# Kernel tuning notes

Hardware: AMD Instinct MI355X
Metric: run time of the kernel (lower is better)

The kernel has to match this reference:

```python
import jax, jax.numpy as jnp
import numpy as np

B, L, H, D = 4, 2048, 12, 64
CHUNK = 128  # chunk size for the causal linear-attention scan
EPS = 1e-6


def setup_inputs() -> dict:
    key = jax.random.key(0)
    kq, kk, kv = jax.random.split(key, 3)
    return {
        "q": jax.random.normal(kq, (B, L, H, D), jnp.float32),
        "k": jax.random.normal(kk, (B, L, H, D), jnp.float32),
        "v": jax.random.normal(kv, (B, L, H, D), jnp.float32),
    }


def _phi(x):
    # elu feature map: elu(x) + 1 (strictly positive)
    return jax.nn.elu(x) + 1.0


def _causal_linear(q, k, v):
    """Chunked causal linear attention numerator.
    out[l] = q[l] @ sum_{s<=l} k[s] (x) v[s].  q,k,v: [N,L,H,D]."""
    n, l, h, d = q.shape
    g = l // CHUNK
    qc = q.reshape(n, g, CHUNK, h, d)
    kc = k.reshape(n, g, CHUNK, h, d)
    vc = v.reshape(n, g, CHUNK, h, d)
    # per-chunk kv outer-product sums -> [N, G, H, D, M]
    kv = jnp.einsum('ngchd,ngchm->nghdm', kc, vc)
    # exclusive prefix sum over chunks (state entering each chunk)
    s_incl = jnp.cumsum(kv, axis=1)
    s_excl = jnp.concatenate([jnp.zeros_like(s_incl[:, :1]), s_incl[:, :-1]], axis=1)
    inter = jnp.einsum('ngchd,nghdm->ngchm', qc, s_excl)
    # intra-chunk causal part
    scores = jnp.einsum('ngchd,ngshd->ngchs', qc, kc)  # [N,G,C,H,C]
    mask = jnp.tril(jnp.ones((CHUNK, CHUNK), scores.dtype))  # s <= c
    scores = scores * mask.reshape(1, 1, CHUNK, 1, CHUNK)
    intra = jnp.einsum('ngchs,ngshm->ngchm', scores, vc)
    return (inter + intra).reshape(n, l, h, -1)


def reference(q, k, v):
    qf = _phi(q)
    kf = _phi(k)
    # normalizer z[n,l,h] = q[l] . cumsum_s<=l k[s]
    z = jnp.einsum('nlhd,nlhd->nlh', qf, jnp.cumsum(kf, axis=1)) + EPS
    num = _causal_linear(qf, kf, v)
    return num / z[..., None]
```

## Files before the change

### kernel.cpp

```cpp
#include <hip/hip_runtime.h>

#define NB 4
#define LL 2048
#define NH 12
#define DD 64
#define CB 64
#define NG (LL/CB)
#define SS (DD*DD + DD)

typedef short bf16x8 __attribute__((ext_vector_type(8)));
typedef float f32x4  __attribute__((ext_vector_type(4)));

#define SWZ(row, x) ((x) ^ (((row) & 7) << 4))

__device__ __forceinline__ float phi(float x) {
    return x > 0.0f ? x + 1.0f : __expf(x);
}
__device__ __forceinline__ unsigned f2bf1(float x) {
    union { float f; unsigned u; } v; v.f = x;
    return (v.u + 0x7FFFu + ((v.u >> 16) & 1u)) >> 16;
}
__device__ __forceinline__ unsigned packbf(float a, float b) {
    return f2bf1(a) | (f2bf1(b) << 16);
}
__device__ __forceinline__ float bf2f(unsigned short u) {
    union { unsigned u; float f; } v; v.u = ((unsigned)u) << 16; return v.f;
}

__global__ __launch_bounds__(256) void la_chunk_sums(
    const float* __restrict__ kin, const float* __restrict__ vin,
    float* __restrict__ ws)
{
    __shared__ __align__(16) char sm[16384];
    const int bid = blockIdx.x;
    const int g  = bid & (NG-1);
    const int h  = (bid / NG) % NH;
    const int n  = bid / (NG*NH);
    const int t  = threadIdx.x;
    const int l0 = g * CB;
    const int w   = t >> 6;
    const int l   = t & 63;
    const int gq  = l >> 4;
    const int c16 = l & 15;

    #pragma unroll
    for (int p = 0; p < 4; ++p) {
        const int i = p*256 + t;
        const int r = i >> 4, c4 = i & 15;
        const size_t gidx = ((size_t)((n*LL + l0 + r)*NH + h))*DD + c4*4;
        float4 kk = *(const float4*)(kin + gidx);
        float4 vl = *(const float4*)(vin + gidx);
        const float kf[4] = {phi(kk.x), phi(kk.y), phi(kk.z), phi(kk.w)};
        const float vf[4] = {vl.x, vl.y, vl.z, vl.w};
        #pragma unroll
        for (int j = 0; j < 4; ++j) {
            const int d = c4*4 + j;
            *(unsigned short*)(sm +        d*128 + SWZ(d, 2*r)) = (unsigned short)f2bf1(kf[j]);
            *(unsigned short*)(sm + 8192 + d*128 + SWZ(d, 2*r)) = (unsigned short)f2bf1(vf[j]);
        }
    }
    __syncthreads();

    const int m = 16*w + c16;
    const bf16x8 va0 = *(const bf16x8*)(sm + 8192 + m*128 + SWZ(m,      gq*16));
    const bf16x8 va1 = *(const bf16x8*)(sm + 8192 + m*128 + SWZ(m, 64 + gq*16));
    f32x4 acc[4];
    #pragma unroll
    for (int td = 0; td < 4; ++td) { acc[td][0]=0.f; acc[td][1]=0.f; acc[td][2]=0.f; acc[td][3]=0.f; }
    #pragma unroll
    for (int td = 0; td < 4; ++td) {
        const int d = 16*td + c16;
        const bf16x8 kb0 = *(const bf16x8*)(sm + d*128 + SWZ(d,      gq*16));
        const bf16x8 kb1 = *(const bf16x8*)(sm + d*128 + SWZ(d, 64 + gq*16));
        acc[td] = __builtin_amdgcn_mfma_f32_16x16x32_bf16(va0, kb0, acc[td], 0, 0, 0);
        acc[td] = __builtin_amdgcn_mfma_f32_16x16x32_bf16(va1, kb1, acc[td], 0, 0, 0);
    }
    float* st = ws + (size_t)bid * SS;
    #pragma unroll
    for (int td = 0; td < 4; ++td)
        #pragma unroll
        for (int e = 0; e < 4; ++e) {
            const int mr = 16*w + 4*gq + e;
            st[mr*DD + 16*td + c16] = acc[td][e];
        }
    if (t < DD) {
        float s = 0.f;
        #pragma unroll 8
        for (int r = 0; r < CB; ++r)
            s += bf2f(*(const unsigned short*)(sm + t*128 + SWZ(t, 2*r)));
        st[DD*DD + t] = s;
    }
}

__global__ __launch_bounds__(256) void la_scan(float* __restrict__ ws)
{
    const int nh = blockIdx.x / 5;
    const int sl = blockIdx.x % 5;
    const int t4 = sl*256 + threadIdx.x;
    if (t4 >= SS/4) return;
    float* base = ws + (size_t)nh * NG * SS + (size_t)t4 * 4;

    float4 run = make_float4(0.f, 0.f, 0.f, 0.f);
    #pragma unroll 1
    for (int g4 = 0; g4 < NG; g4 += 4) {
        float4 a0 = *(float4*)(base + (size_t)(g4+0)*SS);
        float4 a1 = *(float4*)(base + (size_t)(g4+1)*SS);
        float4 a2 = *(float4*)(base + (size_t)(g4+2)*SS);
        float4 a3 = *(float4*)(base + (size_t)(g4+3)*SS);
        *(float4*)(base + (size_t)(g4+0)*SS) = run;
        run.x += a0.x; run.y += a0.y; run.z += a0.z; run.w += a0.w;
        *(float4*)(base + (size_t)(g4+1)*SS) = run;
        run.x += a1.x; run.y += a1.y; run.z += a1.z; run.w += a1.w;
        *(float4*)(base + (size_t)(g4+2)*SS) = run;
        run.x += a2.x; run.y += a2.y; run.z += a2.z; run.w += a2.w;
        *(float4*)(base + (size_t)(g4+3)*SS) = run;
        run.x += a3.x; run.y += a3.y; run.z += a3.z; run.w += a3.w;
    }
}

#define SM_Q   0
#define SM_K   8192
#define SM_VT  16384
#define SM_STX 24576
#define SM_KSX 32768
#define SM_ZL  33024
#define SM_BYTES 33280

__global__ __launch_bounds__(256) void la_output(
    const float* __restrict__ qin, const float* __restrict__ kin,
    const float* __restrict__ vin, const float* __restrict__ ws,
    float* __restrict__ out)
{
    __shared__ __align__(16) char sm[SM_BYTES];
    const int bid = blockIdx.x;
    const int g  = bid & (NG-1);
    const int h  = (bid / NG) % NH;
    const int n  = bid / (NG*NH);
    const int t  = threadIdx.x;
    const int l0 = g * CB;
    const int w   = t >> 6;
    const int l   = t & 63;
    const int gq  = l >> 4;
    const int c16 = l & 15;

    #pragma unroll
    for (int p = 0; p < 4; ++p) {
        const int i = p*256 + t;
        const int row = i >> 4, c4 = i & 15;
        const size_t gidx = ((size_t)((n*LL + l0 + row)*NH + h))*DD + c4*4;
        float4 qq = *(const float4*)(qin + gidx);
        float4 kk = *(const float4*)(kin + gidx);
        float4 vl = *(const float4*)(vin + gidx);
        uint2 qp; qp.x = packbf(phi(qq.x), phi(qq.y)); qp.y = packbf(phi(qq.z), phi(qq.w));
        uint2 kp; kp.x = packbf(phi(kk.x), phi(kk.y)); kp.y = packbf(phi(kk.z), phi(kk.w));
        *(uint2*)(sm + SM_Q + row*128 + SWZ(row, c4*8)) = qp;
        *(uint2*)(sm + SM_K + row*128 + SWZ(row, c4*8)) = kp;
        const float vf[4] = {vl.x, vl.y, vl.z, vl.w};
        #pragma unroll
        for (int j = 0; j < 4; ++j) {
            const int m = c4*4 + j;
            *(unsigned short*)(sm + SM_VT + m*128 + SWZ(m, 2*row)) = (unsigned short)f2bf1(vf[j]);
        }
    }
    const float* stt = ws + (size_t)bid * SS;
    #pragma unroll
    for (int p = 0; p < 4; ++p) {
        const int i = p*256 + t;
        const int m = i >> 4, c4 = i & 15;
        const float4 sv = *(const float4*)(stt + m*DD + c4*4);
        uint2 sp; sp.x = packbf(sv.x, sv.y); sp.y = packbf(sv.z, sv.w);
        *(uint2*)(sm + SM_STX + m*128 + SWZ(m, c4*8)) = sp;
    }
    if (t < DD) ((float*)(sm + SM_KSX))[t] = stt[DD*DD + t];
    __syncthreads();

    const int c = 16*w + c16;
    const bf16x8 qf0 = *(const bf16x8*)(sm + SM_Q + c*128 + SWZ(c,      gq*16));
    const bf16x8 qf1 = *(const bf16x8*)(sm + SM_Q + c*128 + SWZ(c, 64 + gq*16));

    f32x4 sreg[4];
    #pragma unroll
    for (int tr = 0; tr < 4; ++tr) {
        const int r = 16*tr + c16;
        const bf16x8 ka0 = *(const bf16x8*)(sm + SM_K + r*128 + SWZ(r,      gq*16));
        const bf16x8 ka1 = *(const bf16x8*)(sm + SM_K + r*128 + SWZ(r, 64 + gq*16));
        f32x4 a; a[0]=0.f; a[1]=0.f; a[2]=0.f; a[3]=0.f;
        a = __builtin_amdgcn_mfma_f32_16x16x32_bf16(ka0, qf0, a, 0, 0, 0);
        a = __builtin_amdgcn_mfma_f32_16x16x32_bf16(ka1, qf1, a, 0, 0, 0);
        sreg[tr] = a;
    }
    float z = 0.f;
    #pragma unroll
    for (int tr = 0; tr < 4; ++tr)
        #pragma unroll
        for (int e = 0; e < 4; ++e) {
            const int rr = 16*tr + 4*gq + e;
            if (rr <= c) z += sreg[tr][e]; else sreg[tr][e] = 0.f;
        }
    #pragma unroll
    for (int dd = 0; dd < 16; ++dd) {
        const int d = 16*gq + dd;
        const float qv = bf2f(*(const unsigned short*)(sm + SM_Q + c*128 + SWZ(c, 2*d)));
        z += qv * ((const float*)(sm + SM_KSX))[d];
    }
    z += __shfl_xor(z, 16);
    z += __shfl_xor(z, 32);
    __syncthreads();

    #pragma unroll
    for (int tr = 0; tr < 4; ++tr) {
        uint2 sp; sp.x = packbf(sreg[tr][0], sreg[tr][1]); sp.y = packbf(sreg[tr][2], sreg[tr][3]);
        *(uint2*)(sm + SM_K + c*128 + SWZ(c, 32*tr + 8*gq)) = sp;
    }
    if (gq == 0) ((float*)(sm + SM_ZL))[c] = z;
    __syncthreads();

    const bf16x8 sf0 = *(const bf16x8*)(sm + SM_K + c*128 + SWZ(c,      gq*16));
    const bf16x8 sf1 = *(const bf16x8*)(sm + SM_K + c*128 + SWZ(c, 64 + gq*16));
    f32x4 acc[4];
    #pragma unroll
    for (int tm = 0; tm < 4; ++tm) { acc[tm][0]=0.f; acc[tm][1]=0.f; acc[tm][2]=0.f; acc[tm][3]=0.f; }
    #pragma unroll
    for (int tm = 0; tm < 4; ++tm) {
        const int m = 16*tm + c16;
        const bf16x8 vf0 = *(const bf16x8*)(sm + SM_VT + m*128 + SWZ(m,      gq*16));
        const bf16x8 vf1 = *(const bf16x8*)(sm + SM_VT + m*128 + SWZ(m, 64 + gq*16));
        acc[tm] = __builtin_amdgcn_mfma_f32_16x16x32_bf16(sf0, vf0, acc[tm], 0, 0, 0);
        acc[tm] = __builtin_amdgcn_mfma_f32_16x16x32_bf16(sf1, vf1, acc[tm], 0, 0, 0);
        const bf16x8 st0 = *(const bf16x8*)(sm + SM_STX + m*128 + SWZ(m,      gq*16));
        const bf16x8 st1 = *(const bf16x8*)(sm + SM_STX + m*128 + SWZ(m, 64 + gq*16));
        acc[tm] = __builtin_amdgcn_mfma_f32_16x16x32_bf16(qf0, st0, acc[tm], 0, 0, 0);
        acc[tm] = __builtin_amdgcn_mfma_f32_16x16x32_bf16(qf1, st1, acc[tm], 0, 0, 0);
    }

    float zinv[4];
    #pragma unroll
    for (int e = 0; e < 4; ++e) {
        const float zr = ((const float*)(sm + SM_ZL))[16*w + 4*gq + e];
        zinv[e] = 1.0f / (zr + 1e-6f);
    }
    #pragma unroll
    for (int tm = 0; tm < 4; ++tm)
        #pragma unroll
        for (int e = 0; e < 4; ++e) {
            const int cr = 16*w + 4*gq + e;
            const int m  = 16*tm + c16;
            out[((size_t)((n*LL + l0 + cr)*NH + h))*DD + m] = acc[tm][e] * zinv[e];
        }
}

extern "C" void kernel_launch(void* const* d_in, const int* in_sizes, int n_in,
                              void* d_out, int out_size, void* d_ws, size_t ws_size,
                              hipStream_t stream) {
    const float* q = (const float*)d_in[0];
    const float* k = (const float*)d_in[1];
    const float* v = (const float*)d_in[2];
    float* out = (float*)d_out;
    float* ws  = (float*)d_ws;

    const int nblk = NB * NH * NG;
    la_chunk_sums<<<nblk, 256, 0, stream>>>(k, v, ws);
    la_scan<<<NB*NH*5, 256, 0, stream>>>(ws);
    la_output<<<nblk, 256, 0, stream>>>(q, k, v, ws, out);
}
```

Measured before the change: 49.53 us.

## Double chunk size, store chunk states as bf16, compute key sums via MFMA

Raises the chunk length from 64 to 128, which halves the number of chunk states. Per-chunk KV states are now written and scanned in bf16 instead of fp32, cutting workspace traffic in the scan and output kernels. Key column sums are computed with an MFMA against a ones vector instead of a serial loop. The output kernel moves to 512 threads with larger shared memory, and the bf16 running-state writes in the scan add rounding error to the accumulated state.

```diff
diff --git a/kernel.cpp b/kernel.cpp
--- a/kernel.cpp
+++ b/kernel.cpp
@@ -4,14 +4,17 @@
 #define LL 2048
 #define NH 12
 #define DD 64
-#define CB 64
+#define CB 128
 #define NG (LL/CB)
-#define SS (DD*DD + DD)
+#define NBH (NB*NH)
+#define ST_BYTES (DD*DD*2)
+#define KS_BASE_BYTES ((size_t)NBH*NG*ST_BYTES)
 
 typedef short bf16x8 __attribute__((ext_vector_type(8)));
 typedef float f32x4  __attribute__((ext_vector_type(4)));
 
-#define SWZ(row, x) ((x) ^ (((row) & 7) << 4))
+#define SWZ8(row, x)  ((x) ^ (((row) & 7) << 4))
+#define SWZ16(row, x) ((x) ^ (((row) & 15) << 4))
 
 __device__ __forceinline__ float phi(float x) {
     return x > 0.0f ? x + 1.0f : __expf(x);
@@ -26,25 +29,36 @@
 __device__ __forceinline__ float bf2f(unsigned short u) {
     union { unsigned u; float f; } v; v.u = ((unsigned)u) << 16; return v.f;
 }
+__device__ __forceinline__ void addbf8(float* run, uint4 a) {
+    const unsigned u[4] = {a.x, a.y, a.z, a.w};
+    #pragma unroll
+    for (int i = 0; i < 4; ++i) {
+        run[2*i+0] += bf2f((unsigned short)(u[i] & 0xffffu));
+        run[2*i+1] += bf2f((unsigned short)(u[i] >> 16));
+    }
+}
+__device__ __forceinline__ uint4 pack8(const float* run) {
+    uint4 s;
+    s.x = packbf(run[0], run[1]); s.y = packbf(run[2], run[3]);
+    s.z = packbf(run[4], run[5]); s.w = packbf(run[6], run[7]);
+    return s;
+}
 
 __global__ __launch_bounds__(256) void la_chunk_sums(
     const float* __restrict__ kin, const float* __restrict__ vin,
-    float* __restrict__ ws)
+    char* __restrict__ wsb)
 {
-    __shared__ __align__(16) char sm[16384];
+    __shared__ __align__(16) char sm[32768];
     const int bid = blockIdx.x;
-    const int g  = bid & (NG-1);
-    const int h  = (bid / NG) % NH;
-    const int n  = bid / (NG*NH);
-    const int t  = threadIdx.x;
+    const int g = bid & (NG-1);
+    const int h = (bid >> 4) % NH;
+    const int n = bid / (NG*NH);
+    const int t = threadIdx.x;
     const int l0 = g * CB;
-    const int w   = t >> 6;
-    const int l   = t & 63;
-    const int gq  = l >> 4;
-    const int c16 = l & 15;
-
-    #pragma unroll
-    for (int p = 0; p < 4; ++p) {
+    const int w = t >> 6, l = t & 63, gq = l >> 4, c16 = l & 15;
+
+    #pragma unroll
+    for (int p = 0; p < 8; ++p) {
         const int i = p*256 + t;
         const int r = i >> 4, c4 = i & 15;
         const size_t gidx = ((size_t)((n*LL + l0 + r)*NH + h))*DD + c4*4;
@@ -55,135 +69,160 @@
         #pragma unroll
         for (int j = 0; j < 4; ++j) {
             const int d = c4*4 + j;
-            *(unsigned short*)(sm +        d*128 + SWZ(d, 2*r)) = (unsigned short)f2bf1(kf[j]);
-            *(unsigned short*)(sm + 8192 + d*128 + SWZ(d, 2*r)) = (unsigned short)f2bf1(vf[j]);
+            *(unsigned short*)(sm +         d*256 + SWZ16(d, 2*r)) = (unsigned short)f2bf1(kf[j]);
+            *(unsigned short*)(sm + 16384 + d*256 + SWZ16(d, 2*r)) = (unsigned short)f2bf1(vf[j]);
         }
     }
     __syncthreads();
 
     const int m = 16*w + c16;
-    const bf16x8 va0 = *(const bf16x8*)(sm + 8192 + m*128 + SWZ(m,      gq*16));
-    const bf16x8 va1 = *(const bf16x8*)(sm + 8192 + m*128 + SWZ(m, 64 + gq*16));
-    f32x4 acc[4];
-    #pragma unroll
-    for (int td = 0; td < 4; ++td) { acc[td][0]=0.f; acc[td][1]=0.f; acc[td][2]=0.f; acc[td][3]=0.f; }
+    bf16x8 va[4];
+    #pragma unroll
+    for (int ks = 0; ks < 4; ++ks)
+        va[ks] = *(const bf16x8*)(sm + 16384 + m*256 + SWZ16(m, 64*ks + 16*gq));
+    const short one = (short)0x3F80;
+    const bf16x8 ones = {one, one, one, one, one, one, one, one};
+
+    f32x4 acc[4], ksa[4];
+    #pragma unroll
+    for (int td = 0; td < 4; ++td) {
+        acc[td][0]=0.f; acc[td][1]=0.f; acc[td][2]=0.f; acc[td][3]=0.f;
+        ksa[td][0]=0.f; ksa[td][1]=0.f; ksa[td][2]=0.f; ksa[td][3]=0.f;
+    }
     #pragma unroll
     for (int td = 0; td < 4; ++td) {
         const int d = 16*td + c16;
-        const bf16x8 kb0 = *(const bf16x8*)(sm + d*128 + SWZ(d,      gq*16));
-        const bf16x8 kb1 = *(const bf16x8*)(sm + d*128 + SWZ(d, 64 + gq*16));
-        acc[td] = __builtin_amdgcn_mfma_f32_16x16x32_bf16(va0, kb0, acc[td], 0, 0, 0);
-        acc[td] = __builtin_amdgcn_mfma_f32_16x16x32_bf16(va1, kb1, acc[td], 0, 0, 0);
-    }
-    float* st = ws + (size_t)bid * SS;
+        #pragma unroll
+        for (int ks = 0; ks < 4; ++ks) {
+            const bf16x8 kb = *(const bf16x8*)(sm + d*256 + SWZ16(d, 64*ks + 16*gq));
+            acc[td] = __builtin_amdgcn_mfma_f32_16x16x32_bf16(va[ks], kb, acc[td], 0, 0, 0);
+            ksa[td] = __builtin_amdgcn_mfma_f32_16x16x32_bf16(ones,  kb, ksa[td], 0, 0, 0);
+        }
+    }
+    __syncthreads();
+
     #pragma unroll
     for (int td = 0; td < 4; ++td)
         #pragma unroll
         for (int e = 0; e < 4; ++e) {
             const int mr = 16*w + 4*gq + e;
-            st[mr*DD + 16*td + c16] = acc[td][e];
-        }
-    if (t < DD) {
-        float s = 0.f;
-        #pragma unroll 8
-        for (int r = 0; r < CB; ++r)
-            s += bf2f(*(const unsigned short*)(sm + t*128 + SWZ(t, 2*r)));
-        st[DD*DD + t] = s;
-    }
-}
-
-__global__ __launch_bounds__(256) void la_scan(float* __restrict__ ws)
+            const int d  = 16*td + c16;
+            *(unsigned short*)(sm + mr*128 + SWZ8(mr, 2*d)) = (unsigned short)f2bf1(acc[td][e]);
+        }
+    if (w == 0 && gq == 0) {
+        float* ksw = (float*)(wsb + KS_BASE_BYTES) + (size_t)((n*NH + h)*NG + g)*DD;
+        #pragma unroll
+        for (int td = 0; td < 4; ++td)
+            ksw[16*td + c16] = ksa[td][0];
+    }
+    __syncthreads();
+
+    char* stg = wsb + (size_t)((n*NH + h)*NG + g)*ST_BYTES;
+    #pragma unroll
+    for (int p = 0; p < 2; ++p) {
+        const int i = p*256 + t;
+        const int mr = i >> 3, cc = i & 7;
+        *(uint4*)(stg + mr*128 + cc*16) = *(const uint4*)(sm + mr*128 + SWZ8(mr, cc*16));
+    }
+}
+
+__global__ __launch_bounds__(256) void la_scan(char* __restrict__ wsb)
 {
-    const int nh = blockIdx.x / 5;
-    const int sl = blockIdx.x % 5;
-    const int t4 = sl*256 + threadIdx.x;
-    if (t4 >= SS/4) return;
-    float* base = ws + (size_t)nh * NG * SS + (size_t)t4 * 4;
-
-    float4 run = make_float4(0.f, 0.f, 0.f, 0.f);
-    #pragma unroll 1
-    for (int g4 = 0; g4 < NG; g4 += 4) {
-        float4 a0 = *(float4*)(base + (size_t)(g4+0)*SS);
-        float4 a1 = *(float4*)(base + (size_t)(g4+1)*SS);
-        float4 a2 = *(float4*)(base + (size_t)(g4+2)*SS);
-        float4 a3 = *(float4*)(base + (size_t)(g4+3)*SS);
-        *(float4*)(base + (size_t)(g4+0)*SS) = run;
-        run.x += a0.x; run.y += a0.y; run.z += a0.z; run.w += a0.w;
-        *(float4*)(base + (size_t)(g4+1)*SS) = run;
-        run.x += a1.x; run.y += a1.y; run.z += a1.z; run.w += a1.w;
-        *(float4*)(base + (size_t)(g4+2)*SS) = run;
-        run.x += a2.x; run.y += a2.y; run.z += a2.z; run.w += a2.w;
-        *(float4*)(base + (size_t)(g4+3)*SS) = run;
-        run.x += a3.x; run.y += a3.y; run.z += a3.z; run.w += a3.w;
+    const int nh = blockIdx.x / 3;
+    const int sl = blockIdx.x % 3;
+    const int t  = threadIdx.x;
+    if (sl < 2) {
+        const int t4 = sl*256 + t;
+        char* base = wsb + (size_t)nh * NG * ST_BYTES + (size_t)t4 * 16;
+        float run[8];
+        #pragma unroll
+        for (int i = 0; i < 8; ++i) run[i] = 0.f;
+        #pragma unroll
+        for (int g2 = 0; g2 < NG; g2 += 2) {
+            uint4 a0 = *(uint4*)(base + (size_t)(g2+0)*ST_BYTES);
+            uint4 a1 = *(uint4*)(base + (size_t)(g2+1)*ST_BYTES);
+            *(uint4*)(base + (size_t)(g2+0)*ST_BYTES) = pack8(run);
+            addbf8(run, a0);
+            *(uint4*)(base + (size_t)(g2+1)*ST_BYTES) = pack8(run);
+            addbf8(run, a1);
+        }
+    } else if (t < DD) {
+        float* base = (float*)(wsb + KS_BASE_BYTES) + (size_t)nh * NG * DD + t;
+        float run = 0.f;
+        #pragma unroll
+        for (int g4 = 0; g4 < NG; g4 += 4) {
+            float a0 = base[(g4+0)*DD], a1 = base[(g4+1)*DD];
+            float a2 = base[(g4+2)*DD], a3 = base[(g4+3)*DD];
+            base[(g4+0)*DD] = run; run += a0;
+            base[(g4+1)*DD] = run; run += a1;
+            base[(g4+2)*DD] = run; run += a2;
+            base[(g4+3)*DD] = run; run += a3;
+        }
     }
 }
 
 #define SM_Q   0
-#define SM_K   8192
-#define SM_VT  16384
-#define SM_STX 24576
-#define SM_KSX 32768
-#define SM_ZL  33024
-#define SM_BYTES 33280
-
-__global__ __launch_bounds__(256) void la_output(
+#define SM_K   16384
+#define SM_S   0
+#define SM_VT  32768
+#define SM_STX 49152
+#define SM_KSX 57344
+#define SM_ZL  57600
+#define SM_BYTES 58112
+
+__global__ __launch_bounds__(512) void la_output(
     const float* __restrict__ qin, const float* __restrict__ kin,
-    const float* __restrict__ vin, const float* __restrict__ ws,
+    const float* __restrict__ vin, const char* __restrict__ wsb,
     float* __restrict__ out)
 {
     __shared__ __align__(16) char sm[SM_BYTES];
     const int bid = blockIdx.x;
-    const int g  = bid & (NG-1);
-    const int h  = (bid / NG) % NH;
-    const int n  = bid / (NG*NH);
-    const int t  = threadIdx.x;
+    const int g = bid & (NG-1);
+    const int h = (bid >> 4) % NH;
+    const int n = bid / (NG*NH);
+    const int t = threadIdx.x;
     const int l0 = g * CB;
-    const int w   = t >> 6;
-    const int l   = t & 63;
-    const int gq  = l >> 4;
-    const int c16 = l & 15;
+    const int w = t >> 6, l = t & 63, gq = l >> 4, c16 = l & 15;
+    const int c = 16*w + c16;
 
     #pragma unroll
     for (int p = 0; p < 4; ++p) {
-        const int i = p*256 + t;
-        const int row = i >> 4, c4 = i & 15;
-        const size_t gidx = ((size_t)((n*LL + l0 + row)*NH + h))*DD + c4*4;
+        const int i = p*512 + t;
+        const int r = i >> 4, c4 = i & 15;
+        const size_t gidx = ((size_t)((n*LL + l0 + r)*NH + h))*DD + c4*4;
         float4 qq = *(const float4*)(qin + gidx);
         float4 kk = *(const float4*)(kin + gidx);
         float4 vl = *(const float4*)(vin + gidx);
         uint2 qp; qp.x = packbf(phi(qq.x), phi(qq.y)); qp.y = packbf(phi(qq.z), phi(qq.w));
         uint2 kp; kp.x = packbf(phi(kk.x), phi(kk.y)); kp.y = packbf(phi(kk.z), phi(kk.w));
-        *(uint2*)(sm + SM_Q + row*128 + SWZ(row, c4*8)) = qp;
-        *(uint2*)(sm + SM_K + row*128 + SWZ(row, c4*8)) = kp;
+        *(uint2*)(sm + SM_Q + r*128 + SWZ8(r, c4*8)) = qp;
+        *(uint2*)(sm + SM_K + r*128 + SWZ8(r, c4*8)) = kp;
         const float vf[4] = {vl.x, vl.y, vl.z, vl.w};
         #pragma unroll
         for (int j = 0; j < 4; ++j) {
             const int m = c4*4 + j;
-            *(unsigned short*)(sm + SM_VT + m*128 + SWZ(m, 2*row)) = (unsigned short)f2bf1(vf[j]);
-        }
-    }
-    const float* stt = ws + (size_t)bid * SS;
-    #pragma unroll
-    for (int p = 0; p < 4; ++p) {
-        const int i = p*256 + t;
-        const int m = i >> 4, c4 = i & 15;
-        const float4 sv = *(const float4*)(stt + m*DD + c4*4);
-        uint2 sp; sp.x = packbf(sv.x, sv.y); sp.y = packbf(sv.z, sv.w);
-        *(uint2*)(sm + SM_STX + m*128 + SWZ(m, c4*8)) = sp;
-    }
-    if (t < DD) ((float*)(sm + SM_KSX))[t] = stt[DD*DD + t];
-    __syncthreads();
-
-    const int c = 16*w + c16;
-    const bf16x8 qf0 = *(const bf16x8*)(sm + SM_Q + c*128 + SWZ(c,      gq*16));
-    const bf16x8 qf1 = *(const bf16x8*)(sm + SM_Q + c*128 + SWZ(c, 64 + gq*16));
-
-    f32x4 sreg[4];
-    #pragma unroll
-    for (int tr = 0; tr < 4; ++tr) {
+            *(unsigned short*)(sm + SM_VT + m*256 + SWZ16(m, 2*r)) = (unsigned short)f2bf1(vf[j]);
+        }
+    }
+    {
+        const char* stg = wsb + (size_t)((n*NH + h)*NG + g)*ST_BYTES;
+        const int mr = t >> 3, cc = t & 7;
+        *(uint4*)(sm + SM_STX + mr*128 + SWZ8(mr, cc*16)) = *(const uint4*)(stg + mr*128 + cc*16);
+    }
+    if (t < DD)
+        ((float*)(sm + SM_KSX))[t] =
+            ((const float*)(wsb + KS_BASE_BYTES))[(size_t)((n*NH + h)*NG + g)*DD + t];
+    __syncthreads();
+
+    const bf16x8 qf0 = *(const bf16x8*)(sm + SM_Q + c*128 + SWZ8(c, 16*gq));
+    const bf16x8 qf1 = *(const bf16x8*)(sm + SM_Q + c*128 + SWZ8(c, 64 + 16*gq));
+
+    f32x4 sreg[8];
+    #pragma unroll
+    for (int tr = 0; tr < 8; ++tr) {
         const int r = 16*tr + c16;
-        const bf16x8 ka0 = *(const bf16x8*)(sm + SM_K + r*128 + SWZ(r,      gq*16));
-        const bf16x8 ka1 = *(const bf16x8*)(sm + SM_K + r*128 + SWZ(r, 64 + gq*16));
+        const bf16x8 ka0 = *(const bf16x8*)(sm + SM_K + r*128 + SWZ8(r, 16*gq));
+        const bf16x8 ka1 = *(const bf16x8*)(sm + SM_K + r*128 + SWZ8(r, 64 + 16*gq));
         f32x4 a; a[0]=0.f; a[1]=0.f; a[2]=0.f; a[3]=0.f;
         a = __builtin_amdgcn_mfma_f32_16x16x32_bf16(ka0, qf0, a, 0, 0, 0);
         a = __builtin_amdgcn_mfma_f32_16x16x32_bf16(ka1, qf1, a, 0, 0, 0);
@@ -191,44 +230,49 @@
     }
     float z = 0.f;
     #pragma unroll
-    for (int tr = 0; tr < 4; ++tr)
+    for (int tr = 0; tr < 8; ++tr)
         #pragma unroll
         for (int e = 0; e < 4; ++e) {
             const int rr = 16*tr + 4*gq + e;
             if (rr <= c) z += sreg[tr][e]; else sreg[tr][e] = 0.f;
         }
-    #pragma unroll
-    for (int dd = 0; dd < 16; ++dd) {
-        const int d = 16*gq + dd;
-        const float qv = bf2f(*(const unsigned short*)(sm + SM_Q + c*128 + SWZ(c, 2*d)));
-        z += qv * ((const float*)(sm + SM_KSX))[d];
+    {
+        const float* ksxf = (const float*)(sm + SM_KSX);
+        #pragma unroll
+        for (int i = 0; i < 8; ++i) {
+            z += bf2f((unsigned short)qf0[i]) * ksxf[8*gq + i];
+            z += bf2f((unsigned short)qf1[i]) * ksxf[32 + 8*gq + i];
+        }
     }
     z += __shfl_xor(z, 16);
     z += __shfl_xor(z, 32);
     __syncthreads();
 
     #pragma unroll
-    for (int tr = 0; tr < 4; ++tr) {
+    for (int tr = 0; tr < 8; ++tr) {
         uint2 sp; sp.x = packbf(sreg[tr][0], sreg[tr][1]); sp.y = packbf(sreg[tr][2], sreg[tr][3]);
-        *(uint2*)(sm + SM_K + c*128 + SWZ(c, 32*tr + 8*gq)) = sp;
+        *(uint2*)(sm + SM_S + c*256 + SWZ16(c, 32*tr + 8*gq)) = sp;
     }
     if (gq == 0) ((float*)(sm + SM_ZL))[c] = z;
     __syncthreads();
 
-    const bf16x8 sf0 = *(const bf16x8*)(sm + SM_K + c*128 + SWZ(c,      gq*16));
-    const bf16x8 sf1 = *(const bf16x8*)(sm + SM_K + c*128 + SWZ(c, 64 + gq*16));
+    bf16x8 sf[4];
+    #pragma unroll
+    for (int ks = 0; ks < 4; ++ks)
+        sf[ks] = *(const bf16x8*)(sm + SM_S + c*256 + SWZ16(c, 64*ks + 16*gq));
     f32x4 acc[4];
     #pragma unroll
     for (int tm = 0; tm < 4; ++tm) { acc[tm][0]=0.f; acc[tm][1]=0.f; acc[tm][2]=0.f; acc[tm][3]=0.f; }
     #pragma unroll
     for (int tm = 0; tm < 4; ++tm) {
         const int m = 16*tm + c16;
-        const bf16x8 vf0 = *(const bf16x8*)(sm + SM_VT + m*128 + SWZ(m,      gq*16));
-        const bf16x8 vf1 = *(const bf16x8*)(sm + SM_VT + m*128 + SWZ(m, 64 + gq*16));
-        acc[tm] = __builtin_amdgcn_mfma_f32_16x16x32_bf16(sf0, vf0, acc[tm], 0, 0, 0);
-        acc[tm] = __builtin_amdgcn_mfma_f32_16x16x32_bf16(sf1, vf1, acc[tm], 0, 0, 0);
-        const bf16x8 st0 = *(const bf16x8*)(sm + SM_STX + m*128 + SWZ(m,      gq*16));
-        const bf16x8 st1 = *(const bf16x8*)(sm + SM_STX + m*128 + SWZ(m, 64 + gq*16));
+        #pragma unroll
+        for (int ks = 0; ks < 4; ++ks) {
+            const bf16x8 vf = *(const bf16x8*)(sm + SM_VT + m*256 + SWZ16(m, 64*ks + 16*gq));
+            acc[tm] = __builtin_amdgcn_mfma_f32_16x16x32_bf16(sf[ks], vf, acc[tm], 0, 0, 0);
+        }
+        const bf16x8 st0 = *(const bf16x8*)(sm + SM_STX + m*128 + SWZ8(m, 16*gq));
+        const bf16x8 st1 = *(const bf16x8*)(sm + SM_STX + m*128 + SWZ8(m, 64 + 16*gq));
         acc[tm] = __builtin_amdgcn_mfma_f32_16x16x32_bf16(qf0, st0, acc[tm], 0, 0, 0);
         acc[tm] = __builtin_amdgcn_mfma_f32_16x16x32_bf16(qf1, st1, acc[tm], 0, 0, 0);
     }
@@ -256,10 +300,10 @@
     const float* k = (const float*)d_in[1];
     const float* v = (const float*)d_in[2];
     float* out = (float*)d_out;
-    float* ws  = (float*)d_ws;
+    char* wsb  = (char*)d_ws;
 
     const int nblk = NB * NH * NG;
-    la_chunk_sums<<<nblk, 256, 0, stream>>>(k, v, ws);
-    la_scan<<<NB*NH*5, 256, 0, stream>>>(ws);
-    la_output<<<nblk, 256, 0, stream>>>(q, k, v, ws, out);
-}
+    la_chunk_sums<<<nblk, 256, 0, stream>>>(k, v, wsb);
+    la_scan<<<NBH*3, 256, 0, stream>>>(wsb);
+    la_output<<<nblk, 512, 0, stream>>>(q, k, v, wsb, out);
+}
```

After: 40.94 us. -17.4%, faster.
